# Kernel tuning notes

Measured on AMD Instinct MI355X. Metric: run time of the kernel, lower is better.

The kernel has to match this reference:

```python
import jax, jax.numpy as jnp
import numpy as np

B, H, W, C, NB = 3, 256, 256, 16, 4
EPS = 1e-3  # keras BatchNormalization default epsilon


def _conv(x, w, b):
    y = jax.lax.conv_general_dilated(x, w, (1, 1), 'SAME',
                                     dimension_numbers=('NHWC', 'HWIO', 'NHWC'))
    return y + b


def _bn(x, g, be, mu, v):
    # inference-mode batch norm with moving statistics
    return (x - mu) * jax.lax.rsqrt(v + EPS) * g + be


def _extract_patches(x, p, s):
    # tf.image.extract_patches(..., padding='SAME') -> (b, oh, ow, p, p, c)
    b, h, w, c = x.shape
    oh, ow = -(-h // s), -(-w // s)
    pth = max((oh - 1) * s + p - h, 0)
    ptw = max((ow - 1) * s + p - w, 0)
    xp = jnp.pad(x, ((0, 0), (pth // 2, pth - pth // 2), (ptw // 2, ptw - ptw // 2), (0, 0)))
    ri = np.arange(oh)[:, None] * s + np.arange(p)[None, :]  # (oh, p)
    ci = np.arange(ow)[:, None] * s + np.arange(p)[None, :]  # (ow, p)
    return xp[:, ri[:, None, :, None], ci[None, :, None, :], :]


def setup_inputs() -> dict:
    key = jax.random.key(0)
    ks = jax.random.split(key, 4)
    mr = jax.random.normal(ks[0], (B, H, W, C), jnp.float32)
    pet = jax.random.normal(ks[1], (B, H, W, C), jnp.float32)
    W1 = jax.random.normal(ks[2], (3, 3, C, C * NB), jnp.float32) * 0.05
    W2 = jax.random.normal(ks[3], (3, 3, C * NB, C * NB), jnp.float32) * 0.05
    z = jnp.zeros((C * NB,), jnp.float32)
    o = jnp.ones((C * NB,), jnp.float32)
    return dict(mr_features=mr, pet_features=pet,
                W1=W1, b1=z, g1=o, be1=z, mu1=z, v1=o,
                W2=W2, b2=z, g2=o, be2=z, mu2=z, v2=o,
                patch=8, stride=4)


def reference(mr_features, pet_features, W1, b1, g1, be1, mu1, v1,
              W2, b2, g2, be2, mu2, v2, patch, stride):
    px = py = int(patch)
    sx = sy = int(stride)
    bsz, h, w, c = mr_features.shape

    # ---- B_Kernel_Function_Generator ----
    x = jax.nn.relu(_bn(_conv(mr_features, W1, b1), g1, be1, mu1, v1))
    x = _bn(_conv(x, W2, b2), g2, be2, mu2, v2)  # last conv_block: no activation
    nb = x.shape[-1] // c
    x = x.reshape(bsz, h, w, c, nb)
    x = jax.nn.softmax(x, axis=-1)
    b_features = jnp.where(x > 1e-5, x, 0.0)  # mask * x

    # ---- Sparse_Kernel_Matrix_Multiplication ----
    bc, bf = c, nb
    Nx, Ny = h // px, w // py
    lx, ly = px // sx, py // sy
    SNx, SNy = Nx * lx, Ny * ly

    bflat = b_features.reshape(bsz, h, w, bc * bf)
    bp = _extract_patches(bflat, px, sx).reshape(bsz, SNx, SNy, px, py, bc, bf)
    pp = _extract_patches(pet_features, px, sx).reshape(bsz, SNx, SNy, px, py, bc, 1)

    dn = jnp.sum(bp, axis=(3, 4), keepdims=True)              # diagonal norm
    kp = jnp.sum(pp * bp, axis=(3, 4), keepdims=True)         # kernel-weighted PET
    dn_safe = jnp.where(dn == 0, 1.0, dn)
    kn = jnp.where(dn == 0, 0.0, kp / dn_safe) * bp           # divide_no_nan
    kpet = jnp.sum(kn, axis=-1)                               # (b,SNx,SNy,px,py,bc)

    # deinterleave stride phases: kernel_pet[:, i::lx, j::ly] stack
    kp6 = kpet.reshape(bsz, Nx, lx, Ny, ly, px, py, c)
    st = kp6.transpose(4, 2, 0, 1, 3, 5, 6, 7).reshape(lx * ly, bsz, Nx, Ny, px, py, c)
    t = st.transpose(1, 2, 3, 4, 5, 6, 0).reshape(bsz, Nx, Ny, px, py, c, lx, ly)
    t = t.transpose(0, 1, 3, 2, 4, 5, 6, 7).reshape(bsz, Nx * px, Ny * py, c, lx, ly)
    t = t.transpose(4, 5, 0, 1, 2, 3)  # (lx, ly, b, H, W, c)

    # align_patches: roll each shifted copy back into registration, then mean
    rev = t.transpose(2, 3, 4, 5, 0, 1).reshape(bsz, h, w, c, lx * ly)
    rev = rev.transpose(4, 0, 1, 2, 3)  # (lx*ly, b, H, W, c)
    rollx = np.arange(-px // 2 + sx // 2, px // 2 + sx // 2, sx)
    rolly = np.arange(-py // 2 + sy // 2, py // 2 + sy // 2, sy)
    acc = jnp.zeros((bsz, h, w, c), rev.dtype)
    for m in range(lx * ly):  # small fixed set (lx*ly = 4)
        acc = acc + jnp.roll(rev[m], (int(rollx[m % lx]), int(rolly[m // lx])), axis=(1, 2))
    return acc / (lx * ly)
```

## Files before the change

kernel.cpp:

```cpp
#include <hip/hip_runtime.h>

#define EPSB 1e-3f

typedef _Float16 half8 __attribute__((ext_vector_type(8)));
typedef _Float16 half4 __attribute__((ext_vector_type(4)));
typedef _Float16 half2v __attribute__((ext_vector_type(2)));
typedef float f32x4 __attribute__((ext_vector_type(4)));

__global__ __launch_bounds__(256, 4)
void k_prep(const float* __restrict__ W1, const float* __restrict__ W2,
            const float* __restrict__ b1, const float* __restrict__ g1,
            const float* __restrict__ be1, const float* __restrict__ mu1,
            const float* __restrict__ v1,
            const float* __restrict__ b2, const float* __restrict__ g2,
            const float* __restrict__ be2, const float* __restrict__ mu2,
            const float* __restrict__ v2,
            _Float16* __restrict__ W1F, _Float16* __restrict__ W2F,
            float* __restrict__ ST)
{
    int t = blockIdx.x * 256 + threadIdx.x;
    if (t < 5 * 4 * 64 * 8) {
        int k = t & 7, lane = (t >> 3) & 63, snt = t >> 9;
        int s = snt >> 2, ct = snt & 3;
        int quad = lane >> 4, n16 = lane & 15;
        int tap = 2 * s + (quad >> 1);
        int ci  = (quad & 1) * 8 + k;
        int co  = ct * 16 + n16;
        float v = (tap < 9) ? W1[(tap * 16 + ci) * 64 + co] : 0.f;
        W1F[t] = (_Float16)v;
        return;
    }
    t -= 5 * 4 * 64 * 8;
    if (t < 18 * 4 * 64 * 8) {
        int k = t & 7, lane = (t >> 3) & 63, snt = t >> 9;
        int s = snt >> 2, ct = snt & 3;
        int quad = lane >> 4, n16 = lane & 15;
        int tap = s >> 1;
        int ci  = (s & 1) * 32 + quad * 8 + k;
        int co  = ct * 16 + n16;
        W2F[t] = (_Float16)W2[(tap * 64 + ci) * 64 + co];
        return;
    }
    t -= 18 * 4 * 64 * 8;
    if (t < 256) {
        int c = t & 63, sel = t >> 6;
        if (sel == 0)      ST[c]       = g1[c] * rsqrtf(v1[c] + EPSB);
        else if (sel == 1) ST[64 + c]  = (b1[c] - mu1[c]) * (g1[c] * rsqrtf(v1[c] + EPSB)) + be1[c];
        else if (sel == 2) ST[128 + c] = g2[c] * rsqrtf(v2[c] + EPSB);
        else               ST[192 + c] = (b2[c] - mu2[c]) * (g2[c] * rsqrtf(v2[c] + EPSB)) + be2[c];
    }
}

__global__ __launch_bounds__(256, 4)
void k_zero(_Float16* __restrict__ A)
{
    int t = blockIdx.x * 256 + threadIdx.x;
    if (t >= 3 * 1028 * 8) return;
    int b = t / 8224;
    int rem = t - b * 8224;
    int px = rem >> 3, seg = rem & 7;
    int row, col;
    if (px < 258)      { row = 0;        col = px; }
    else if (px < 516) { row = 257;      col = px - 258; }
    else if (px < 772) { row = px - 515; col = 0; }
    else               { row = px - 771; col = 257; }
    int4 z = {0, 0, 0, 0};
    *(int4*)(A + (((size_t)b * 258 + row) * 258 + col) * 64 + seg * 8) = z;
}

__global__ __launch_bounds__(256, 3)
void k_conv1(const float* __restrict__ mr, const _Float16* __restrict__ W1F,
             const float* __restrict__ ST, _Float16* __restrict__ A)
{
    __shared__ __align__(16) _Float16 sM[4 * 64 * 72];
    const int tid = threadIdx.x;
    const int b  = blockIdx.y;
    const int r0 = (blockIdx.x >> 2) * 4;
    const int q0 = (blockIdx.x & 3) * 64;
    const int w = tid >> 6, lane = tid & 63;
    const int n16 = lane & 15, quad = lane >> 4;
    const int r = r0 + w;
    const _Float16* W1l = W1F + lane * 8;

    f32x4 acc[4][4];
    #pragma unroll
    for (int i = 0; i < 4; ++i)
        #pragma unroll
        for (int j = 0; j < 4; ++j) acc[i][j] = (f32x4){0.f, 0.f, 0.f, 0.f};

    #pragma unroll
    for (int s = 0; s < 5; ++s) {
        half8 wf[4];
        #pragma unroll
        for (int ct = 0; ct < 4; ++ct)
            wf[ct] = *(const half8*)(W1l + (s * 4 + ct) * 512);
        int tap  = 2 * s + (quad >> 1);
        int tapc = tap > 8 ? 8 : tap;
        int dy = tapc / 3, dx = tapc % 3;
        int rr = r + dy - 1;
        bool rok = (unsigned)rr < 256u;
        #pragma unroll
        for (int qt = 0; qt < 4; ++qt) {
            int qg = q0 + qt * 16 + n16 + dx - 1;
            bool ok = rok && ((unsigned)qg < 256u);
            const float* src = mr + (((b * 256 + (ok ? rr : 0)) * 256 + (ok ? qg : 0)) * 16
                                     + (quad & 1) * 8);
            float4 v0 = *(const float4*)src;
            float4 v1 = *(const float4*)(src + 4);
            half8 pf = ok ? (half8){(_Float16)v0.x, (_Float16)v0.y, (_Float16)v0.z, (_Float16)v0.w,
                                    (_Float16)v1.x, (_Float16)v1.y, (_Float16)v1.z, (_Float16)v1.w}
                          : (half8)(_Float16)0.f;
            #pragma unroll
            for (int ct = 0; ct < 4; ++ct)
                acc[qt][ct] = __builtin_amdgcn_mfma_f32_16x16x32_f16(wf[ct], pf, acc[qt][ct], 0, 0, 0);
        }
    }

    #pragma unroll
    for (int ct = 0; ct < 4; ++ct) {
        int co0 = ct * 16 + quad * 4;
        f32x4 sc = *(const f32x4*)&ST[co0];
        f32x4 sh = *(const f32x4*)&ST[64 + co0];
        #pragma unroll
        for (int qt = 0; qt < 4; ++qt) {
            half4 h;
            #pragma unroll
            for (int j = 0; j < 4; ++j)
                h[j] = (_Float16)fmaxf(acc[qt][ct][j] * sc[j] + sh[j], 0.f);
            *(half4*)(&sM[w * 4608 + (qt * 16 + n16) * 72 + co0]) = h;
        }
    }
    __syncthreads();

    for (int idx = tid; idx < 2048; idx += 256) {
        int rl = idx >> 9, rest = idx & 511;
        int ql = rest >> 3, seg = rest & 7;
        int4 v = *(const int4*)&sM[rl * 4608 + ql * 72 + seg * 8];
        *(int4*)(A + (((size_t)b * 258 + (r0 + rl + 1)) * 258 + (q0 + ql + 1)) * 64 + seg * 8) = v;
    }
}

__global__ __launch_bounds__(256, 3)
void k_conv2(const _Float16* __restrict__ A, const _Float16* __restrict__ W2F,
             const float* __restrict__ ST, const float* __restrict__ pet,
             _Float16* __restrict__ BF, _Float16* __restrict__ S2h)
{
    __shared__ __align__(16) _Float16 sM[4 * 64 * 72];
    const int tid = threadIdx.x;
    const int b  = blockIdx.y;
    const int r0 = (blockIdx.x >> 2) * 4;
    const int q0 = (blockIdx.x & 3) * 64;
    const int w = tid >> 6, lane = tid & 63;
    const int n16 = lane & 15, quad = lane >> 4;
    const int r = r0 + w;
    const _Float16* W2l = W2F + lane * 8;

    const _Float16* pb[3][4];
    #pragma unroll
    for (int dy = 0; dy < 3; ++dy)
        #pragma unroll
        for (int qt = 0; qt < 4; ++qt)
            pb[dy][qt] = A + (((size_t)b * 258 + r + dy) * 258 + (q0 + qt * 16 + n16)) * 64
                           + quad * 8;

    f32x4 acc[4][4];
    #pragma unroll
    for (int i = 0; i < 4; ++i)
        #pragma unroll
        for (int j = 0; j < 4; ++j) acc[i][j] = (f32x4){0.f, 0.f, 0.f, 0.f};

    #pragma unroll
    for (int s = 0; s < 18; ++s) {
        const int tap = s >> 1;
        const int dy = tap / 3, dx = tap % 3;
        const int cio = (s & 1) * 32;
        half8 wf[4], pf[4];
        #pragma unroll
        for (int ct = 0; ct < 4; ++ct)
            wf[ct] = *(const half8*)(W2l + (s * 4 + ct) * 512);
        #pragma unroll
        for (int qt = 0; qt < 4; ++qt)
            pf[qt] = *(const half8*)(pb[dy][qt] + dx * 64 + cio);
        #pragma unroll
        for (int qt = 0; qt < 4; ++qt)
            #pragma unroll
            for (int ct = 0; ct < 4; ++ct)
                acc[qt][ct] = __builtin_amdgcn_mfma_f32_16x16x32_f16(wf[ct], pf[qt], acc[qt][ct], 0, 0, 0);
    }

    #pragma unroll
    for (int ct = 0; ct < 4; ++ct) {
        int co0 = ct * 16 + quad * 4;
        f32x4 sc = *(const f32x4*)&ST[128 + co0];
        f32x4 sh = *(const f32x4*)&ST[192 + co0];
        #pragma unroll
        for (int qt = 0; qt < 4; ++qt) {
            float z0 = acc[qt][ct][0] * sc[0] + sh[0];
            float z1 = acc[qt][ct][1] * sc[1] + sh[1];
            float z2 = acc[qt][ct][2] * sc[2] + sh[2];
            float z3 = acc[qt][ct][3] * sc[3] + sh[3];
            float mx = fmaxf(fmaxf(z0, z1), fmaxf(z2, z3));
            float e0 = __expf(z0 - mx), e1 = __expf(z1 - mx);
            float e2 = __expf(z2 - mx), e3 = __expf(z3 - mx);
            float inv = __builtin_amdgcn_rcpf((e0 + e1) + (e2 + e3));
            float p0 = e0 * inv, p1 = e1 * inv, p2 = e2 * inv, p3 = e3 * inv;
            half4 h;
            h[0] = (_Float16)(p0 > 1e-5f ? p0 : 0.f);
            h[1] = (_Float16)(p1 > 1e-5f ? p1 : 0.f);
            h[2] = (_Float16)(p2 > 1e-5f ? p2 : 0.f);
            h[3] = (_Float16)(p3 > 1e-5f ? p3 : 0.f);
            *(half4*)(&sM[w * 4608 + (qt * 16 + n16) * 72 + co0]) = h;
        }
    }
    __syncthreads();

    for (int idx = tid; idx < 2048; idx += 256) {
        int rl = idx >> 9, rest = idx & 511;
        int ql = rest >> 3, seg = rest & 7;
        int4 v = *(const int4*)&sM[rl * 4608 + ql * 72 + seg * 8];
        *(int4*)(BF + (((b * 256 + r0 + rl) * 256 + q0 + ql) * 64 + seg * 8)) = v;
    }

    const int qp = tid >> 3, chg = tid & 7;
    #pragma unroll
    for (int cr = 0; cr < 2; ++cr) {
        float dn[8], kp[8];
        #pragma unroll
        for (int j = 0; j < 8; ++j) { dn[j] = 0.f; kp[j] = 0.f; }
        #pragma unroll
        for (int u = 0; u < 2; ++u)
            #pragma unroll
            for (int v = 0; v < 2; ++v) {
                int rl = 2 * cr + u, ql = 2 * qp + v;
                half8 bf = *(const half8*)(&sM[rl * 4608 + ql * 72 + chg * 8]);
                float2 p2 = *(const float2*)(pet + ((b * 256 + r0 + rl) * 256 + q0 + ql) * 16 + chg * 2);
                #pragma unroll
                for (int j = 0; j < 8; ++j) {
                    float bv = (float)bf[j];
                    dn[j] += bv;
                    kp[j] = fmaf((j < 4) ? p2.x : p2.y, bv, kp[j]);
                }
            }
        _Float16* o = S2h + 2 * ((size_t)(((b * 128 + (r0 >> 1) + cr) * 128 + (q0 >> 1) + qp) * 64) + chg * 8);
        #pragma unroll
        for (int m = 0; m < 2; ++m) {
            half8 h;
            #pragma unroll
            for (int j = 0; j < 4; ++j) {
                h[2 * j]     = (_Float16)dn[4 * m + j];
                h[2 * j + 1] = (_Float16)kp[4 * m + j];
            }
            *(half8*)(o + 8 * m) = h;
        }
    }
}

__global__ __launch_bounds__(256, 4)
void k_ratio(const _Float16* __restrict__ S2h, float* __restrict__ RATIO)
{
    int t = blockIdx.x * 256 + threadIdx.x;
    int cf = t & 63;
    int j  = (t >> 6) & 63;
    int i  = (t >> 12) & 63;
    int b  = t >> 18;
    float dn = 0.f, kp = 0.f;
    #pragma unroll
    for (int u = 0; u < 4; ++u) {
        int r2 = 2 * i - 1 + u;
        if ((unsigned)r2 >= 128u) continue;
        #pragma unroll
        for (int v = 0; v < 4; ++v) {
            int q2 = 2 * j - 1 + v;
            if ((unsigned)q2 >= 128u) continue;
            half2v s = *(const half2v*)(S2h + 2 * (((b * 128 + r2) * 128 + q2) * 64 + cf));
            dn += (float)s[0];
            kp += (float)s[1];
        }
    }
    RATIO[t] = (dn == 0.f) ? 0.f : 0.25f * kp * __builtin_amdgcn_rcpf(dn);
}

__global__ __launch_bounds__(256, 4)
void k_out(const _Float16* __restrict__ BF, const float* __restrict__ RATIO,
           float* __restrict__ out)
{
    __shared__ __align__(16) float sU[64 * 68];
    const int tid = threadIdx.x;
    const int r = blockIdx.x & 255;
    const int b = blockIdx.x >> 8;

    const int i0 = (r <= 253) ? 2 * ((r + 2) >> 3)       : -1;
    const int i1 = (r >= 2)   ? 2 * ((r - 2) >> 3) + 1   : -1;

    for (int idx = tid; idx < 1024; idx += 256) {
        int j = idx >> 4, c4 = idx & 15;
        float4 a = make_float4(0.f, 0.f, 0.f, 0.f);
        if (i0 >= 0) a = *(const float4*)&RATIO[(((b * 64 + i0) * 64 + j) << 6) + 4 * c4];
        float4 bb = make_float4(0.f, 0.f, 0.f, 0.f);
        if (i1 >= 0) bb = *(const float4*)&RATIO[(((b * 64 + i1) * 64 + j) << 6) + 4 * c4];
        *(float4*)&sU[j * 68 + 4 * c4] = make_float4(a.x + bb.x, a.y + bb.y, a.z + bb.z, a.w + bb.w);
    }
    __syncthreads();

    const int q = tid;
    const int j0 = (q <= 253) ? 2 * ((q + 2) >> 3)     : -1;
    const int j1 = (q >= 2)   ? 2 * ((q - 2) >> 3) + 1 : -1;

    const half8* bfp = (const half8*)(BF + ((size_t)(b * 256 + r) * 256 + q) * 64);
    float o[16];
    #pragma unroll
    for (int c = 0; c < 16; ++c) o[c] = 0.f;

    #pragma unroll
    for (int c2 = 0; c2 < 8; ++c2) {
        half8 bf8 = bfp[c2];
        float s0 = 0.f, s1 = 0.f;
        #pragma unroll
        for (int pj = 0; pj < 2; ++pj) {
            int jj = pj ? j1 : j0;
            if (jj < 0) continue;
            const float* up = &sU[jj * 68 + 8 * c2];
            s0 += (float)bf8[0] * up[0] + (float)bf8[1] * up[1]
                + (float)bf8[2] * up[2] + (float)bf8[3] * up[3];
            s1 += (float)bf8[4] * up[4] + (float)bf8[5] * up[5]
                + (float)bf8[6] * up[6] + (float)bf8[7] * up[7];
        }
        o[2 * c2]     = s0;
        o[2 * c2 + 1] = s1;
    }
    float* op = out + ((size_t)(b * 256 + r) * 256 + q) * 16;
    #pragma unroll
    for (int m = 0; m < 4; ++m)
        *(float4*)(op + 4 * m) = make_float4(o[4*m], o[4*m+1], o[4*m+2], o[4*m+3]);
}

extern "C" void kernel_launch(void* const* d_in, const int* in_sizes, int n_in,
                              void* d_out, int out_size, void* d_ws, size_t ws_size,
                              hipStream_t stream) {
    const float* mr  = (const float*)d_in[0];
    const float* pet = (const float*)d_in[1];
    const float* W1  = (const float*)d_in[2];
    const float* b1  = (const float*)d_in[3];
    const float* g1  = (const float*)d_in[4];
    const float* be1 = (const float*)d_in[5];
    const float* mu1 = (const float*)d_in[6];
    const float* v1  = (const float*)d_in[7];
    const float* W2  = (const float*)d_in[8];
    const float* b2  = (const float*)d_in[9];
    const float* g2  = (const float*)d_in[10];
    const float* be2 = (const float*)d_in[11];
    const float* mu2 = (const float*)d_in[12];
    const float* v2  = (const float*)d_in[13];

    char* ws = (char*)d_ws;
    _Float16* A     = (_Float16*)(ws);
    _Float16* BF    = (_Float16*)(ws + 25560576);
    _Float16* S2h   = (_Float16*)(ws + 50726400);
    float*    RATIO = (float*)(ws + 63309312);
    _Float16* W1F   = (_Float16*)(ws + 66455040);
    _Float16* W2F   = (_Float16*)(ws + 66475520);
    float*    ST    = (float*)(ws + 66549248);
    float*    out   = (float*)d_out;

    dim3 blk(256);
    k_prep<<<185, blk, 0, stream>>>(W1, W2, b1, g1, be1, mu1, v1,
                                    b2, g2, be2, mu2, v2, W1F, W2F, ST);
    k_zero<<<97, blk, 0, stream>>>(A);
    k_conv1<<<dim3(256, 3), blk, 0, stream>>>(mr, W1F, ST, A);
    k_conv2<<<dim3(256, 3), blk, 0, stream>>>(A, W2F, ST, pet, BF, S2h);
    k_ratio<<<3072, blk, 0, stream>>>(S2h, RATIO);
    k_out<<<768, blk, 0, stream>>>(BF, RATIO, out);
}
```

Before: 178.2 us.

## Split conv blocks over output-channel halves and merge zero-fill into prep kernel

Each conv block now covers 2 rows instead of 4, with the four waves split as 2 rows × 2 output-channel halves. This halves the accumulators per wave and the shared memory per block, doubles the grid, and raises launch bounds to 4 blocks per CU for higher occupancy and better load balance. The border zeroing of the padded activation buffer is folded into the prep kernel, which removes one launch. The cost is that each input patch fragment is now loaded by two waves, so input load traffic per MFMA roughly doubles.

```diff
diff --git a/kernel.cpp b/kernel.cpp
--- a/kernel.cpp
+++ b/kernel.cpp
@@ -16,7 +16,7 @@
             const float* __restrict__ be2, const float* __restrict__ mu2,
             const float* __restrict__ v2,
             _Float16* __restrict__ W1F, _Float16* __restrict__ W2F,
-            float* __restrict__ ST)
+            float* __restrict__ ST, _Float16* __restrict__ A)
 {
     int t = blockIdx.x * 256 + threadIdx.x;
     if (t < 5 * 4 * 64 * 8) {
@@ -48,52 +48,50 @@
         else if (sel == 1) ST[64 + c]  = (b1[c] - mu1[c]) * (g1[c] * rsqrtf(v1[c] + EPSB)) + be1[c];
         else if (sel == 2) ST[128 + c] = g2[c] * rsqrtf(v2[c] + EPSB);
         else               ST[192 + c] = (b2[c] - mu2[c]) * (g2[c] * rsqrtf(v2[c] + EPSB)) + be2[c];
-    }
-}
-
-__global__ __launch_bounds__(256, 4)
-void k_zero(_Float16* __restrict__ A)
-{
-    int t = blockIdx.x * 256 + threadIdx.x;
-    if (t >= 3 * 1028 * 8) return;
-    int b = t / 8224;
-    int rem = t - b * 8224;
-    int px = rem >> 3, seg = rem & 7;
-    int row, col;
-    if (px < 258)      { row = 0;        col = px; }
-    else if (px < 516) { row = 257;      col = px - 258; }
-    else if (px < 772) { row = px - 515; col = 0; }
-    else               { row = px - 771; col = 257; }
-    int4 z = {0, 0, 0, 0};
-    *(int4*)(A + (((size_t)b * 258 + row) * 258 + col) * 64 + seg * 8) = z;
-}
-
-__global__ __launch_bounds__(256, 3)
+        return;
+    }
+    t -= 256;
+    if (t < 3 * 1028 * 8) {
+        int b = t / 8224;
+        int rem = t - b * 8224;
+        int px = rem >> 3, seg = rem & 7;
+        int row, col;
+        if (px < 258)      { row = 0;        col = px; }
+        else if (px < 516) { row = 257;      col = px - 258; }
+        else if (px < 772) { row = px - 515; col = 0; }
+        else               { row = px - 771; col = 257; }
+        int4 z = {0, 0, 0, 0};
+        *(int4*)(A + (((size_t)b * 258 + row) * 258 + col) * 64 + seg * 8) = z;
+    }
+}
+
+__global__ __launch_bounds__(256, 4)
 void k_conv1(const float* __restrict__ mr, const _Float16* __restrict__ W1F,
              const float* __restrict__ ST, _Float16* __restrict__ A)
 {
-    __shared__ __align__(16) _Float16 sM[4 * 64 * 72];
+    __shared__ __align__(16) _Float16 sM[2 * 64 * 72];
     const int tid = threadIdx.x;
     const int b  = blockIdx.y;
-    const int r0 = (blockIdx.x >> 2) * 4;
+    const int r0 = (blockIdx.x >> 2) * 2;
     const int q0 = (blockIdx.x & 3) * 64;
     const int w = tid >> 6, lane = tid & 63;
     const int n16 = lane & 15, quad = lane >> 4;
-    const int r = r0 + w;
+    const int rl = w & 1, coh = w >> 1;
+    const int r = r0 + rl;
     const _Float16* W1l = W1F + lane * 8;
 
-    f32x4 acc[4][4];
+    f32x4 acc[4][2];
     #pragma unroll
     for (int i = 0; i < 4; ++i)
         #pragma unroll
-        for (int j = 0; j < 4; ++j) acc[i][j] = (f32x4){0.f, 0.f, 0.f, 0.f};
+        for (int j = 0; j < 2; ++j) acc[i][j] = (f32x4){0.f, 0.f, 0.f, 0.f};
 
     #pragma unroll
     for (int s = 0; s < 5; ++s) {
-        half8 wf[4];
-        #pragma unroll
-        for (int ct = 0; ct < 4; ++ct)
-            wf[ct] = *(const half8*)(W1l + (s * 4 + ct) * 512);
+        half8 wf[2];
+        #pragma unroll
+        for (int c = 0; c < 2; ++c)
+            wf[c] = *(const half8*)(W1l + ((s * 4 + 2 * coh + c) * 512));
         int tap  = 2 * s + (quad >> 1);
         int tapc = tap > 8 ? 8 : tap;
         int dy = tapc / 3, dx = tapc % 3;
@@ -111,14 +109,14 @@
                                     (_Float16)v1.x, (_Float16)v1.y, (_Float16)v1.z, (_Float16)v1.w}
                           : (half8)(_Float16)0.f;
             #pragma unroll
-            for (int ct = 0; ct < 4; ++ct)
-                acc[qt][ct] = __builtin_amdgcn_mfma_f32_16x16x32_f16(wf[ct], pf, acc[qt][ct], 0, 0, 0);
-        }
-    }
-
-    #pragma unroll
-    for (int ct = 0; ct < 4; ++ct) {
-        int co0 = ct * 16 + quad * 4;
+            for (int c = 0; c < 2; ++c)
+                acc[qt][c] = __builtin_amdgcn_mfma_f32_16x16x32_f16(wf[c], pf, acc[qt][c], 0, 0, 0);
+        }
+    }
+
+    #pragma unroll
+    for (int c = 0; c < 2; ++c) {
+        int co0 = (2 * coh + c) * 16 + quad * 4;
         f32x4 sc = *(const f32x4*)&ST[co0];
         f32x4 sh = *(const f32x4*)&ST[64 + co0];
         #pragma unroll
@@ -126,33 +124,34 @@
             half4 h;
             #pragma unroll
             for (int j = 0; j < 4; ++j)
-                h[j] = (_Float16)fmaxf(acc[qt][ct][j] * sc[j] + sh[j], 0.f);
-            *(half4*)(&sM[w * 4608 + (qt * 16 + n16) * 72 + co0]) = h;
+                h[j] = (_Float16)fmaxf(acc[qt][c][j] * sc[j] + sh[j], 0.f);
+            *(half4*)(&sM[rl * 4608 + (qt * 16 + n16) * 72 + co0]) = h;
         }
     }
     __syncthreads();
 
-    for (int idx = tid; idx < 2048; idx += 256) {
-        int rl = idx >> 9, rest = idx & 511;
+    for (int idx = tid; idx < 1024; idx += 256) {
+        int rl2 = idx >> 9, rest = idx & 511;
         int ql = rest >> 3, seg = rest & 7;
-        int4 v = *(const int4*)&sM[rl * 4608 + ql * 72 + seg * 8];
-        *(int4*)(A + (((size_t)b * 258 + (r0 + rl + 1)) * 258 + (q0 + ql + 1)) * 64 + seg * 8) = v;
-    }
-}
-
-__global__ __launch_bounds__(256, 3)
+        int4 v = *(const int4*)&sM[rl2 * 4608 + ql * 72 + seg * 8];
+        *(int4*)(A + (((size_t)b * 258 + (r0 + rl2 + 1)) * 258 + (q0 + ql + 1)) * 64 + seg * 8) = v;
+    }
+}
+
+__global__ __launch_bounds__(256, 4)
 void k_conv2(const _Float16* __restrict__ A, const _Float16* __restrict__ W2F,
              const float* __restrict__ ST, const float* __restrict__ pet,
              _Float16* __restrict__ BF, _Float16* __restrict__ S2h)
 {
-    __shared__ __align__(16) _Float16 sM[4 * 64 * 72];
+    __shared__ __align__(16) _Float16 sM[2 * 64 * 72];
     const int tid = threadIdx.x;
     const int b  = blockIdx.y;
-    const int r0 = (blockIdx.x >> 2) * 4;
+    const int r0 = (blockIdx.x >> 2) * 2;
     const int q0 = (blockIdx.x & 3) * 64;
     const int w = tid >> 6, lane = tid & 63;
     const int n16 = lane & 15, quad = lane >> 4;
-    const int r = r0 + w;
+    const int rl = w & 1, coh = w >> 1;
+    const int r = r0 + rl;
     const _Float16* W2l = W2F + lane * 8;
 
     const _Float16* pb[3][4];
@@ -163,42 +162,42 @@
             pb[dy][qt] = A + (((size_t)b * 258 + r + dy) * 258 + (q0 + qt * 16 + n16)) * 64
                            + quad * 8;
 
-    f32x4 acc[4][4];
+    f32x4 acc[4][2];
     #pragma unroll
     for (int i = 0; i < 4; ++i)
         #pragma unroll
-        for (int j = 0; j < 4; ++j) acc[i][j] = (f32x4){0.f, 0.f, 0.f, 0.f};
+        for (int j = 0; j < 2; ++j) acc[i][j] = (f32x4){0.f, 0.f, 0.f, 0.f};
 
     #pragma unroll
     for (int s = 0; s < 18; ++s) {
         const int tap = s >> 1;
         const int dy = tap / 3, dx = tap % 3;
         const int cio = (s & 1) * 32;
-        half8 wf[4], pf[4];
-        #pragma unroll
-        for (int ct = 0; ct < 4; ++ct)
-            wf[ct] = *(const half8*)(W2l + (s * 4 + ct) * 512);
+        half8 wf[2], pf[4];
+        #pragma unroll
+        for (int c = 0; c < 2; ++c)
+            wf[c] = *(const half8*)(W2l + ((s * 4 + 2 * coh + c) * 512));
         #pragma unroll
         for (int qt = 0; qt < 4; ++qt)
             pf[qt] = *(const half8*)(pb[dy][qt] + dx * 64 + cio);
         #pragma unroll
         for (int qt = 0; qt < 4; ++qt)
             #pragma unroll
-            for (int ct = 0; ct < 4; ++ct)
-                acc[qt][ct] = __builtin_amdgcn_mfma_f32_16x16x32_f16(wf[ct], pf[qt], acc[qt][ct], 0, 0, 0);
-    }
-
-    #pragma unroll
-    for (int ct = 0; ct < 4; ++ct) {
-        int co0 = ct * 16 + quad * 4;
+            for (int c = 0; c < 2; ++c)
+                acc[qt][c] = __builtin_amdgcn_mfma_f32_16x16x32_f16(wf[c], pf[qt], acc[qt][c], 0, 0, 0);
+    }
+
+    #pragma unroll
+    for (int c = 0; c < 2; ++c) {
+        int co0 = (2 * coh + c) * 16 + quad * 4;
         f32x4 sc = *(const f32x4*)&ST[128 + co0];
         f32x4 sh = *(const f32x4*)&ST[192 + co0];
         #pragma unroll
         for (int qt = 0; qt < 4; ++qt) {
-            float z0 = acc[qt][ct][0] * sc[0] + sh[0];
-            float z1 = acc[qt][ct][1] * sc[1] + sh[1];
-            float z2 = acc[qt][ct][2] * sc[2] + sh[2];
-            float z3 = acc[qt][ct][3] * sc[3] + sh[3];
+            float z0 = acc[qt][c][0] * sc[0] + sh[0];
+            float z1 = acc[qt][c][1] * sc[1] + sh[1];
+            float z2 = acc[qt][c][2] * sc[2] + sh[2];
+            float z3 = acc[qt][c][3] * sc[3] + sh[3];
             float mx = fmaxf(fmaxf(z0, z1), fmaxf(z2, z3));
             float e0 = __expf(z0 - mx), e1 = __expf(z1 - mx);
             float e2 = __expf(z2 - mx), e3 = __expf(z3 - mx);
@@ -209,49 +208,46 @@
             h[1] = (_Float16)(p1 > 1e-5f ? p1 : 0.f);
             h[2] = (_Float16)(p2 > 1e-5f ? p2 : 0.f);
             h[3] = (_Float16)(p3 > 1e-5f ? p3 : 0.f);
-            *(half4*)(&sM[w * 4608 + (qt * 16 + n16) * 72 + co0]) = h;
+            *(half4*)(&sM[rl * 4608 + (qt * 16 + n16) * 72 + co0]) = h;
         }
     }
     __syncthreads();
 
-    for (int idx = tid; idx < 2048; idx += 256) {
-        int rl = idx >> 9, rest = idx & 511;
+    for (int idx = tid; idx < 1024; idx += 256) {
+        int rl2 = idx >> 9, rest = idx & 511;
         int ql = rest >> 3, seg = rest & 7;
-        int4 v = *(const int4*)&sM[rl * 4608 + ql * 72 + seg * 8];
-        *(int4*)(BF + (((b * 256 + r0 + rl) * 256 + q0 + ql) * 64 + seg * 8)) = v;
+        int4 v = *(const int4*)&sM[rl2 * 4608 + ql * 72 + seg * 8];
+        *(int4*)(BF + (((b * 256 + r0 + rl2) * 256 + q0 + ql) * 64 + seg * 8)) = v;
     }
 
     const int qp = tid >> 3, chg = tid & 7;
-    #pragma unroll
-    for (int cr = 0; cr < 2; ++cr) {
-        float dn[8], kp[8];
-        #pragma unroll
-        for (int j = 0; j < 8; ++j) { dn[j] = 0.f; kp[j] = 0.f; }
-        #pragma unroll
-        for (int u = 0; u < 2; ++u)
+    float dn[8], kp[8];
+    #pragma unroll
+    for (int j = 0; j < 8; ++j) { dn[j] = 0.f; kp[j] = 0.f; }
+    #pragma unroll
+    for (int u = 0; u < 2; ++u)
+        #pragma unroll
+        for (int v = 0; v < 2; ++v) {
+            int ql = 2 * qp + v;
+            half8 bf = *(const half8*)(&sM[u * 4608 + ql * 72 + chg * 8]);
+            float2 p2 = *(const float2*)(pet + ((b * 256 + r0 + u) * 256 + q0 + ql) * 16 + chg * 2);
             #pragma unroll
-            for (int v = 0; v < 2; ++v) {
-                int rl = 2 * cr + u, ql = 2 * qp + v;
-                half8 bf = *(const half8*)(&sM[rl * 4608 + ql * 72 + chg * 8]);
-                float2 p2 = *(const float2*)(pet + ((b * 256 + r0 + rl) * 256 + q0 + ql) * 16 + chg * 2);
-                #pragma unroll
-                for (int j = 0; j < 8; ++j) {
-                    float bv = (float)bf[j];
-                    dn[j] += bv;
-                    kp[j] = fmaf((j < 4) ? p2.x : p2.y, bv, kp[j]);
-                }
+            for (int j = 0; j < 8; ++j) {
+                float bv = (float)bf[j];
+                dn[j] += bv;
+                kp[j] = fmaf((j < 4) ? p2.x : p2.y, bv, kp[j]);
             }
-        _Float16* o = S2h + 2 * ((size_t)(((b * 128 + (r0 >> 1) + cr) * 128 + (q0 >> 1) + qp) * 64) + chg * 8);
-        #pragma unroll
-        for (int m = 0; m < 2; ++m) {
-            half8 h;
-            #pragma unroll
-            for (int j = 0; j < 4; ++j) {
-                h[2 * j]     = (_Float16)dn[4 * m + j];
-                h[2 * j + 1] = (_Float16)kp[4 * m + j];
-            }
-            *(half8*)(o + 8 * m) = h;
-        }
+        }
+    _Float16* o = S2h + 2 * ((size_t)(((b * 128 + (r0 >> 1)) * 128 + (q0 >> 1) + qp) * 64) + chg * 8);
+    #pragma unroll
+    for (int m = 0; m < 2; ++m) {
+        half8 h;
+        #pragma unroll
+        for (int j = 0; j < 4; ++j) {
+            h[2 * j]     = (_Float16)dn[4 * m + j];
+            h[2 * j + 1] = (_Float16)kp[4 * m + j];
+        }
+        *(half8*)(o + 8 * m) = h;
     }
 }
 
@@ -363,11 +359,10 @@
     float*    out   = (float*)d_out;
 
     dim3 blk(256);
-    k_prep<<<185, blk, 0, stream>>>(W1, W2, b1, g1, be1, mu1, v1,
-                                    b2, g2, be2, mu2, v2, W1F, W2F, ST);
-    k_zero<<<97, blk, 0, stream>>>(A);
-    k_conv1<<<dim3(256, 3), blk, 0, stream>>>(mr, W1F, ST, A);
-    k_conv2<<<dim3(256, 3), blk, 0, stream>>>(A, W2F, ST, pet, BF, S2h);
+    k_prep<<<282, blk, 0, stream>>>(W1, W2, b1, g1, be1, mu1, v1,
+                                    b2, g2, be2, mu2, v2, W1F, W2F, ST, A);
+    k_conv1<<<dim3(512, 3), blk, 0, stream>>>(mr, W1F, ST, A);
+    k_conv2<<<dim3(512, 3), blk, 0, stream>>>(A, W2F, ST, pet, BF, S2h);
     k_ratio<<<3072, blk, 0, stream>>>(S2h, RATIO);
     k_out<<<768, blk, 0, stream>>>(BF, RATIO, out);
 }
```

Result: slower. 201.6 us (+13.1%).
